# Optimization experiments

Measured on AMD Instinct MI355X. Metric: run time of the kernel, lower is better.

Reference implementation:

```python
import jax, jax.numpy as jnp
import numpy as np

B = 512        # graphs per batch
N_NODES = 64   # nodes per graph
IN_CH = 256
EMBED = 64
TOPK = 20
NEG_SLOPE = 0.2


def setup_inputs() -> dict:
    key = jax.random.key(0)
    ks = jax.random.split(key, 6)
    N = B * N_NODES
    x = jax.random.normal(ks[0], (N, IN_CH), dtype=jnp.float32)
    # fully-connected graph WITH self loops, per graph, sorted source-major
    src = jnp.repeat(jnp.arange(N_NODES, dtype=jnp.int32), N_NODES)  # [n*n]
    dst = jnp.tile(jnp.arange(N_NODES, dtype=jnp.int32), N_NODES)    # [n*n]
    offs = (jnp.arange(B, dtype=jnp.int32) * N_NODES)[:, None]       # [B,1]
    l = (src[None, :] + offs).reshape(-1)
    r = (dst[None, :] + offs).reshape(-1)
    edge_index = jnp.stack([l, r]).astype(jnp.int32)                 # [2, B*n*n]
    batch = jnp.repeat(jnp.arange(B, dtype=jnp.int32), N_NODES)      # [N]
    glorot = lambda k, sh: jax.random.uniform(k, sh, jnp.float32,
                                              -1.0, 1.0) * np.sqrt(6.0 / (sh[0] + sh[-1]))
    Wl = glorot(ks[1], (EMBED, IN_CH))
    bl = jnp.zeros((EMBED,), jnp.float32)
    Wr = glorot(ks[2], (EMBED, IN_CH))
    br = jnp.zeros((EMBED,), jnp.float32)
    att = glorot(ks[3], (1, EMBED))
    return {"x": x, "edge_index": edge_index, "batch": batch,
            "Wl": Wl, "bl": bl, "Wr": Wr, "br": br, "att": att}


def reference(x, edge_index, batch, Wl, bl, Wr, br, att):
    N = x.shape[0]
    x_l = x @ Wl.T + bl                      # [N, D]
    x_r = x @ Wr.T + br                      # [N, D]
    l, r = edge_index[0], edge_index[1]
    # edge gather + GAT-style score
    e = jax.nn.leaky_relu(x_l[l] + x_r[r], negative_slope=NEG_SLOPE)  # [E, D]
    alpha = (e * att[0]).sum(axis=-1)                                  # [E]
    # segment softmax grouped by source node l (each group is non-empty)
    m = jax.ops.segment_max(alpha, l, num_segments=N)
    a = jnp.exp(alpha - m[l])
    s = jax.ops.segment_sum(a, l, num_segments=N)
    a = a / s[l]
    # kNN sparsify: zero the diagonal then per-row topk
    a3 = a.reshape(B, N_NODES, N_NODES)
    a3 = a3 * (1.0 - jnp.eye(N_NODES, dtype=a3.dtype))
    attention, indices = jax.lax.top_k(a3, TOPK)     # [B, n, k] sorted desc
    attention = attention.reshape(-1)                 # [B*n*k]
    offs = (jnp.arange(B, dtype=jnp.int32) * N_NODES)[:, None]
    index_i = (jnp.repeat(jnp.arange(N_NODES, dtype=jnp.int32), TOPK)[None, :]
               + offs).reshape(-1)
    index_j = (indices.astype(jnp.int32)
               + (jnp.arange(B, dtype=jnp.int32) * N_NODES)[:, None, None]).reshape(-1)
    new_edge_index = jnp.stack([index_i, index_j])    # [2, B*n*k]
    return new_edge_index, attention
```

## Files before the change

kernel.cpp:

```cpp
#include <hip/hip_runtime.h>
#include <stdint.h>

#define NGRAPH 512
#define NN 64
#define INCH 256
#define TOPK 20
#define EPR 655360

typedef __attribute__((ext_vector_type(8))) short bf16x8;
typedef __attribute__((ext_vector_type(4))) float f32x4;
typedef __attribute__((ext_vector_type(2))) uint32_t u32x2;

#define XLP   0
#define XRP   2176
#define ALF   4352
#define LISTS 0
#define MROW  8704
#define SROW  8960
#define SLOF  9216
#define SROF  9280
#define ATTO  9344
#define SMEM_DW 9408

static __device__ __forceinline__ uint32_t f2bfbits(float f) {
  uint32_t u = __float_as_uint(f);
  return (u + 0x7FFFu + ((u >> 16) & 1u)) >> 16;
}
static __device__ __forceinline__ uint32_t pk2(float a, float b) {
  return f2bfbits(a) | (f2bfbits(b) << 16);
}
static __device__ __forceinline__ float lo16f(uint32_t p) { return __uint_as_float(p << 16); }
static __device__ __forceinline__ float hi16f(uint32_t p) { return __uint_as_float(p & 0xFFFF0000u); }

__global__ __launch_bounds__(256, 4) void gat_fused(
    const float* __restrict__ x,
    const float* __restrict__ Wl,
    const float* __restrict__ blv,
    const float* __restrict__ Wr,
    const float* __restrict__ brv,
    const float* __restrict__ att,
    float* __restrict__ out)
{
  __shared__ __align__(16) uint32_t smemU[SMEM_DW];
  float* smemF = (float*)smemU;

  const int b    = blockIdx.x;
  const int t    = threadIdx.x;
  const int w    = t >> 6;
  const int lane = t & 63;
  const int quad = lane >> 4;
  const int lo   = lane & 15;
  const int nodeBase = b * NN;

  if (t < 64) smemF[ATTO + t] = att[t];

  f32x4 acc[8];
  #pragma unroll
  for (int ct = 0; ct < 8; ++ct) acc[ct] = (f32x4){0.f, 0.f, 0.f, 0.f};

  const int r0 = w * 16;
  #pragma unroll
  for (int ks = 0; ks < 8; ++ks) {
    const int k0 = ks * 32 + quad * 8;
    const float* ap = x + (size_t)(nodeBase + r0 + lo) * INCH + k0;
    float4 a0 = *(const float4*)ap;
    float4 a1 = *(const float4*)(ap + 4);
    uint4 au = { pk2(a0.x, a0.y), pk2(a0.z, a0.w), pk2(a1.x, a1.y), pk2(a1.z, a1.w) };
    bf16x8 afrag = __builtin_bit_cast(bf16x8, au);
    #pragma unroll
    for (int ct = 0; ct < 8; ++ct) {
      const float* wrow = ((ct < 4) ? Wl : Wr) + (size_t)((ct & 3) * 16 + lo) * INCH + k0;
      float4 b0 = *(const float4*)wrow;
      float4 b1 = *(const float4*)(wrow + 4);
      uint4 bu = { pk2(b0.x, b0.y), pk2(b0.z, b0.w), pk2(b1.x, b1.y), pk2(b1.z, b1.w) };
      bf16x8 bfrag = __builtin_bit_cast(bf16x8, bu);
      acc[ct] = __builtin_amdgcn_mfma_f32_16x16x32_bf16(afrag, bfrag, acc[ct], 0, 0, 0);
    }
  }

  #pragma unroll
  for (int ct = 0; ct < 8; ++ct) {
    const int c = (ct & 3) * 16 + lo;
    const float bias = ((ct < 4) ? blv : brv)[c];
    const int base = ((ct < 4) ? XLP : XRP) + c * 34 + (r0 >> 1) + quad * 2;
    u32x2 v = { pk2(acc[ct][0] + bias, acc[ct][1] + bias),
                pk2(acc[ct][2] + bias, acc[ct][3] + bias) };
    *(u32x2*)&smemU[base] = v;
  }
  __syncthreads();

  if (t < 128) {
    const int i = t & 63;
    const int base = (t < 64) ? XLP : XRP;
    float s = 0.f;
    #pragma unroll 4
    for (int d = 0; d < 64; ++d) {
      uint32_t p = smemU[base + d * 34 + (i >> 1)];
      float v = (i & 1) ? hi16f(p) : lo16f(p);
      s = fmaf(smemF[ATTO + d], v, s);
    }
    smemF[((t < 64) ? SLOF : SROF) + i] = s;
  }
  __syncthreads();

  const int i0 = (t >> 4) * 4;
  const int j0 = (t & 15) * 4;
  float pacc[4][4];
  #pragma unroll
  for (int a = 0; a < 4; ++a)
    #pragma unroll
    for (int c = 0; c < 4; ++c) pacc[a][c] = 0.f;

  #pragma unroll 4
  for (int d = 0; d < 64; ++d) {
    u32x2 pl = *(const u32x2*)&smemU[XLP + d * 34 + (i0 >> 1)];
    u32x2 pr = *(const u32x2*)&smemU[XRP + d * 34 + (j0 >> 1)];
    const float ad = smemF[ATTO + d];
    float xl[4] = { lo16f(pl.x), hi16f(pl.x), lo16f(pl.y), hi16f(pl.y) };
    float xr[4] = { lo16f(pr.x), hi16f(pr.x), lo16f(pr.y), hi16f(pr.y) };
    #pragma unroll
    for (int a = 0; a < 4; ++a) {
      #pragma unroll
      for (int c = 0; c < 4; ++c) {
        float s = xl[a] + xr[c];
        pacc[a][c] = fmaf(ad, fabsf(s), pacc[a][c]);
      }
    }
  }
  {
    f32x4 srv = *(const f32x4*)&smemF[SROF + j0];
    #pragma unroll
    for (int a = 0; a < 4; ++a) {
      const float sl = smemF[SLOF + i0 + a];
      f32x4 v;
      #pragma unroll
      for (int c = 0; c < 4; ++c)
        v[c] = 0.6f * (sl + srv[c]) + 0.4f * pacc[a][c];
      *(f32x4*)&smemF[ALF + (i0 + a) * 68 + j0] = v;
    }
  }
  __syncthreads();

  {
    const int row = t & 63;
    const int seg = t >> 6;
    const int segBase = seg * 16;
    float fr[16];
    *(f32x4*)&fr[0]  = *(const f32x4*)&smemF[ALF + row * 68 + segBase];
    *(f32x4*)&fr[4]  = *(const f32x4*)&smemF[ALF + row * 68 + segBase + 4];
    *(f32x4*)&fr[8]  = *(const f32x4*)&smemF[ALF + row * 68 + segBase + 8];
    *(f32x4*)&fr[12] = *(const f32x4*)&smemF[ALF + row * 68 + segBase + 12];

    float mp = fr[0];
    #pragma unroll
    for (int e = 1; e < 16; ++e) mp = fmaxf(mp, fr[e]);
    float sp = 0.f;
    #pragma unroll
    for (int e = 0; e < 16; ++e) sp += __expf(fr[e] - mp);

    uint32_t tk[16];
    #pragma unroll
    for (int k = 0; k < 16; ++k) tk[k] = 0u;
    #pragma unroll
    for (int e = 0; e < 16; ++e) {
      const int j = segBase + e;
      uint32_t u = __float_as_uint(fr[e]);
      uint32_t key = u ^ ((uint32_t)((int32_t)u >> 31) | 0x80000000u);
      key = (key & 0xFFFFFFC0u) | (uint32_t)(63 - j);
      key = (j == row) ? 0u : key;
      #pragma unroll
      for (int k = 15; k >= 1; --k)
        tk[k] = (key > tk[k]) ? ((key < tk[k - 1]) ? key : tk[k - 1]) : tk[k];
      tk[0] = (key > tk[0]) ? key : tk[0];
    }
    #pragma unroll
    for (int k = 0; k < 16; ++k)
      smemU[LISTS + row * 65 + segBase + k] = tk[k];
    smemF[MROW + seg * 64 + row] = mp;
    smemF[SROW + seg * 64 + row] = sp;
  }
  __syncthreads();

  if (t < 64) {
    const int row = t;
    const int lb = LISTS + row * 65;
    float m01 = fmaxf(smemF[MROW + row], smemF[MROW + 64 + row]);
    float m23 = fmaxf(smemF[MROW + 128 + row], smemF[MROW + 192 + row]);
    float m = fmaxf(m01, m23);
    float S = 0.f;
    #pragma unroll
    for (int p = 0; p < 4; ++p)
      S += smemF[SROW + p * 64 + row] * __expf(smemF[MROW + p * 64 + row] - m);
    const float invS = 1.0f / S;

    uint32_t h0 = smemU[lb + 0], h1 = smemU[lb + 16], h2 = smemU[lb + 32], h3 = smemU[lb + 48];
    int p0 = 0, p1 = 0, p2 = 0, p3 = 0;
    float va[TOPK], vj[TOPK];

    #pragma unroll
    for (int k = 0; k < TOPK; ++k) {
      uint32_t k01 = (h0 > h1) ? h0 : h1;
      uint32_t k23 = (h2 > h3) ? h2 : h3;
      uint32_t key = (k01 > k23) ? k01 : k23;
      const int wsel = (key == h0) ? 0 : (key == h1) ? 1 : (key == h2) ? 2 : 3;

      uint32_t ub = (key & 0x80000000u) ? (key ^ 0x80000000u) : ~key;
      float alpha = __uint_as_float(ub & 0xFFFFFFC0u);
      const int j = 63 - (int)(key & 63u);
      va[k] = __expf(alpha - m) * invS;
      vj[k] = (float)(nodeBase + j);

      int np = ((wsel == 0) ? p0 : (wsel == 1) ? p1 : (wsel == 2) ? p2 : p3) + 1;
      uint32_t hn = (np < 16) ? smemU[lb + wsel * 16 + np] : 0u;
      p0 += (wsel == 0); p1 += (wsel == 1); p2 += (wsel == 2); p3 += (wsel == 3);
      h0 = (wsel == 0) ? hn : h0;
      h1 = (wsel == 1) ? hn : h1;
      h2 = (wsel == 2) ? hn : h2;
      h3 = (wsel == 3) ? hn : h3;
    }

    const int g = nodeBase + row;
    const float vi = (float)g;
    float4* o0 = (float4*)(out + (size_t)g * 20);
    float4* o1 = (float4*)(out + EPR + (size_t)g * 20);
    float4* o2 = (float4*)(out + 2 * (size_t)EPR + (size_t)g * 20);
    const float4 vi4 = { vi, vi, vi, vi };
    #pragma unroll
    for (int kk = 0; kk < 5; ++kk) {
      o0[kk] = vi4;
      o1[kk] = (float4){ vj[4 * kk], vj[4 * kk + 1], vj[4 * kk + 2], vj[4 * kk + 3] };
      o2[kk] = (float4){ va[4 * kk], va[4 * kk + 1], va[4 * kk + 2], va[4 * kk + 3] };
    }
  }
}

extern "C" void kernel_launch(void* const* d_in, const int* in_sizes, int n_in,
                              void* d_out, int out_size, void* d_ws, size_t ws_size,
                              hipStream_t stream) {
  const float* x   = (const float*)d_in[0];
  const float* Wl  = (const float*)d_in[3];
  const float* bl  = (const float*)d_in[4];
  const float* Wr  = (const float*)d_in[5];
  const float* br  = (const float*)d_in[6];
  const float* att = (const float*)d_in[7];
  gat_fused<<<dim3(NGRAPH), dim3(256), 0, stream>>>(x, Wl, bl, Wr, br, att, (float*)d_out);
}
```

Baseline: 138.6 us.

## Prepack weights to bf16 in a pre-kernel and double threads per graph

Adds a small kernel that converts Wl and Wr to packed bf16 once per call, so the main kernel loads ready-made B fragments instead of converting fp32 weights to bf16 in every block. The main kernel now runs 512 threads per graph: half the waves compute x_l and half x_r, and the pairwise score, per-segment top-k and merge stages are split across 8 segments instead of 4. Projected features are kept in fp32 in shared memory rather than bf16, which grows LDS use. The cost is an extra launch, a larger merge over 8 lists, and possibly lower occupancy.

```diff
diff --git a/kernel.cpp b/kernel.cpp
--- a/kernel.cpp
+++ b/kernel.cpp
@@ -9,18 +9,17 @@
 
 typedef __attribute__((ext_vector_type(8))) short bf16x8;
 typedef __attribute__((ext_vector_type(4))) float f32x4;
-typedef __attribute__((ext_vector_type(2))) uint32_t u32x2;
-
-#define XLP   0
-#define XRP   2176
-#define ALF   4352
+
+#define XLF   0
+#define XRF   4352
+#define ALF   8704
 #define LISTS 0
-#define MROW  8704
-#define SROW  8960
-#define SLOF  9216
-#define SROF  9280
-#define ATTO  9344
-#define SMEM_DW 9408
+#define MROW  13056
+#define SROW  13568
+#define SLOF  14080
+#define SROF  14144
+#define ATTO  14208
+#define SMEM_DW 14272
 
 static __device__ __forceinline__ uint32_t f2bfbits(float f) {
   uint32_t u = __float_as_uint(f);
@@ -29,14 +28,21 @@
 static __device__ __forceinline__ uint32_t pk2(float a, float b) {
   return f2bfbits(a) | (f2bfbits(b) << 16);
 }
-static __device__ __forceinline__ float lo16f(uint32_t p) { return __uint_as_float(p << 16); }
-static __device__ __forceinline__ float hi16f(uint32_t p) { return __uint_as_float(p & 0xFFFF0000u); }
-
-__global__ __launch_bounds__(256, 4) void gat_fused(
+
+__global__ __launch_bounds__(256) void wpack(const float* __restrict__ Wl,
+                                             const float* __restrict__ Wr,
+                                             uint32_t* __restrict__ ws) {
+  const int t = blockIdx.x * 256 + threadIdx.x;
+  const float* src = (t < 8192) ? Wl : Wr;
+  const int p = t & 8191;
+  float2 v = *(const float2*)(src + (size_t)p * 2);
+  ws[t] = pk2(v.x, v.y);
+}
+
+__global__ __launch_bounds__(512, 4) void gat_fused(
     const float* __restrict__ x,
-    const float* __restrict__ Wl,
+    const uint32_t* __restrict__ ws,
     const float* __restrict__ blv,
-    const float* __restrict__ Wr,
     const float* __restrict__ brv,
     const float* __restrict__ att,
     float* __restrict__ out)
@@ -54,11 +60,13 @@
 
   if (t < 64) smemF[ATTO + t] = att[t];
 
-  f32x4 acc[8];
+  const int half = w >> 2;
+  const int r0   = (w & 3) * 16;
+  f32x4 acc[4];
   #pragma unroll
-  for (int ct = 0; ct < 8; ++ct) acc[ct] = (f32x4){0.f, 0.f, 0.f, 0.f};
-
-  const int r0 = w * 16;
+  for (int ct = 0; ct < 4; ++ct) acc[ct] = (f32x4){0.f, 0.f, 0.f, 0.f};
+
+  const uint4* wsV = (const uint4*)ws;
   #pragma unroll
   for (int ks = 0; ks < 8; ++ks) {
     const int k0 = ks * 32 + quad * 8;
@@ -68,69 +76,64 @@
     uint4 au = { pk2(a0.x, a0.y), pk2(a0.z, a0.w), pk2(a1.x, a1.y), pk2(a1.z, a1.w) };
     bf16x8 afrag = __builtin_bit_cast(bf16x8, au);
     #pragma unroll
-    for (int ct = 0; ct < 8; ++ct) {
-      const float* wrow = ((ct < 4) ? Wl : Wr) + (size_t)((ct & 3) * 16 + lo) * INCH + k0;
-      float4 b0 = *(const float4*)wrow;
-      float4 b1 = *(const float4*)(wrow + 4);
-      uint4 bu = { pk2(b0.x, b0.y), pk2(b0.z, b0.w), pk2(b1.x, b1.y), pk2(b1.z, b1.w) };
+    for (int ct = 0; ct < 4; ++ct) {
+      const int n = ct * 16 + lo;
+      uint4 bu = wsV[half * 2048 + n * 32 + ks * 4 + quad];
       bf16x8 bfrag = __builtin_bit_cast(bf16x8, bu);
       acc[ct] = __builtin_amdgcn_mfma_f32_16x16x32_bf16(afrag, bfrag, acc[ct], 0, 0, 0);
     }
   }
 
-  #pragma unroll
-  for (int ct = 0; ct < 8; ++ct) {
-    const int c = (ct & 3) * 16 + lo;
-    const float bias = ((ct < 4) ? blv : brv)[c];
-    const int base = ((ct < 4) ? XLP : XRP) + c * 34 + (r0 >> 1) + quad * 2;
-    u32x2 v = { pk2(acc[ct][0] + bias, acc[ct][1] + bias),
-                pk2(acc[ct][2] + bias, acc[ct][3] + bias) };
-    *(u32x2*)&smemU[base] = v;
+  {
+    const int dstBase = half ? XRF : XLF;
+    const float* bias = half ? brv : blv;
+    #pragma unroll
+    for (int ct = 0; ct < 4; ++ct) {
+      const int c = ct * 16 + lo;
+      const float bb = bias[c];
+      f32x4 v = { acc[ct][0] + bb, acc[ct][1] + bb, acc[ct][2] + bb, acc[ct][3] + bb };
+      *(f32x4*)&smemF[dstBase + c * 68 + r0 + quad * 4] = v;
+    }
   }
   __syncthreads();
 
   if (t < 128) {
     const int i = t & 63;
-    const int base = (t < 64) ? XLP : XRP;
+    const int base = (t < 64) ? XLF : XRF;
     float s = 0.f;
-    #pragma unroll 4
-    for (int d = 0; d < 64; ++d) {
-      uint32_t p = smemU[base + d * 34 + (i >> 1)];
-      float v = (i & 1) ? hi16f(p) : lo16f(p);
-      s = fmaf(smemF[ATTO + d], v, s);
-    }
+    #pragma unroll 8
+    for (int d = 0; d < 64; ++d)
+      s = fmaf(smemF[ATTO + d], smemF[base + d * 68 + i], s);
     smemF[((t < 64) ? SLOF : SROF) + i] = s;
   }
   __syncthreads();
 
-  const int i0 = (t >> 4) * 4;
+  const int i0 = (t >> 4) * 2;
   const int j0 = (t & 15) * 4;
-  float pacc[4][4];
+  float pacc[2][4];
   #pragma unroll
-  for (int a = 0; a < 4; ++a)
+  for (int a = 0; a < 2; ++a)
     #pragma unroll
     for (int c = 0; c < 4; ++c) pacc[a][c] = 0.f;
 
   #pragma unroll 4
   for (int d = 0; d < 64; ++d) {
-    u32x2 pl = *(const u32x2*)&smemU[XLP + d * 34 + (i0 >> 1)];
-    u32x2 pr = *(const u32x2*)&smemU[XRP + d * 34 + (j0 >> 1)];
+    float xl0 = smemF[XLF + d * 68 + i0];
+    float xl1 = smemF[XLF + d * 68 + i0 + 1];
+    f32x4 xr  = *(const f32x4*)&smemF[XRF + d * 68 + j0];
     const float ad = smemF[ATTO + d];
-    float xl[4] = { lo16f(pl.x), hi16f(pl.x), lo16f(pl.y), hi16f(pl.y) };
-    float xr[4] = { lo16f(pr.x), hi16f(pr.x), lo16f(pr.y), hi16f(pr.y) };
-    #pragma unroll
-    for (int a = 0; a < 4; ++a) {
-      #pragma unroll
-      for (int c = 0; c < 4; ++c) {
-        float s = xl[a] + xr[c];
-        pacc[a][c] = fmaf(ad, fabsf(s), pacc[a][c]);
-      }
+    #pragma unroll
+    for (int c = 0; c < 4; ++c) {
+      float s0 = xl0 + xr[c];
+      float s1 = xl1 + xr[c];
+      pacc[0][c] = fmaf(ad, fabsf(s0), pacc[0][c]);
+      pacc[1][c] = fmaf(ad, fabsf(s1), pacc[1][c]);
     }
   }
   {
     f32x4 srv = *(const f32x4*)&smemF[SROF + j0];
     #pragma unroll
-    for (int a = 0; a < 4; ++a) {
+    for (int a = 0; a < 2; ++a) {
       const float sl = smemF[SLOF + i0 + a];
       f32x4 v;
       #pragma unroll
@@ -144,38 +147,36 @@
   {
     const int row = t & 63;
     const int seg = t >> 6;
-    const int segBase = seg * 16;
-    float fr[16];
-    *(f32x4*)&fr[0]  = *(const f32x4*)&smemF[ALF + row * 68 + segBase];
-    *(f32x4*)&fr[4]  = *(const f32x4*)&smemF[ALF + row * 68 + segBase + 4];
-    *(f32x4*)&fr[8]  = *(const f32x4*)&smemF[ALF + row * 68 + segBase + 8];
-    *(f32x4*)&fr[12] = *(const f32x4*)&smemF[ALF + row * 68 + segBase + 12];
+    const int cb  = seg * 8;
+    f32x4 f0 = *(const f32x4*)&smemF[ALF + row * 68 + cb];
+    f32x4 f1 = *(const f32x4*)&smemF[ALF + row * 68 + cb + 4];
+    float fr[8] = { f0[0], f0[1], f0[2], f0[3], f1[0], f1[1], f1[2], f1[3] };
 
     float mp = fr[0];
     #pragma unroll
-    for (int e = 1; e < 16; ++e) mp = fmaxf(mp, fr[e]);
+    for (int e = 1; e < 8; ++e) mp = fmaxf(mp, fr[e]);
     float sp = 0.f;
     #pragma unroll
-    for (int e = 0; e < 16; ++e) sp += __expf(fr[e] - mp);
-
-    uint32_t tk[16];
-    #pragma unroll
-    for (int k = 0; k < 16; ++k) tk[k] = 0u;
-    #pragma unroll
-    for (int e = 0; e < 16; ++e) {
-      const int j = segBase + e;
+    for (int e = 0; e < 8; ++e) sp += __expf(fr[e] - mp);
+
+    uint32_t tk[8];
+    #pragma unroll
+    for (int k = 0; k < 8; ++k) tk[k] = 0u;
+    #pragma unroll
+    for (int e = 0; e < 8; ++e) {
+      const int j = cb + e;
       uint32_t u = __float_as_uint(fr[e]);
       uint32_t key = u ^ ((uint32_t)((int32_t)u >> 31) | 0x80000000u);
       key = (key & 0xFFFFFFC0u) | (uint32_t)(63 - j);
       key = (j == row) ? 0u : key;
       #pragma unroll
-      for (int k = 15; k >= 1; --k)
+      for (int k = 7; k >= 1; --k)
         tk[k] = (key > tk[k]) ? ((key < tk[k - 1]) ? key : tk[k - 1]) : tk[k];
       tk[0] = (key > tk[0]) ? key : tk[0];
     }
     #pragma unroll
-    for (int k = 0; k < 16; ++k)
-      smemU[LISTS + row * 65 + segBase + k] = tk[k];
+    for (int k = 0; k < 8; ++k)
+      smemU[LISTS + row * 65 + cb + k] = tk[k];
     smemF[MROW + seg * 64 + row] = mp;
     smemF[SROW + seg * 64 + row] = sp;
   }
@@ -184,25 +185,32 @@
   if (t < 64) {
     const int row = t;
     const int lb = LISTS + row * 65;
-    float m01 = fmaxf(smemF[MROW + row], smemF[MROW + 64 + row]);
-    float m23 = fmaxf(smemF[MROW + 128 + row], smemF[MROW + 192 + row]);
-    float m = fmaxf(m01, m23);
+    float m = smemF[MROW + row];
+    #pragma unroll
+    for (int p = 1; p < 8; ++p) m = fmaxf(m, smemF[MROW + p * 64 + row]);
     float S = 0.f;
     #pragma unroll
-    for (int p = 0; p < 4; ++p)
+    for (int p = 0; p < 8; ++p)
       S += smemF[SROW + p * 64 + row] * __expf(smemF[MROW + p * 64 + row] - m);
     const float invS = 1.0f / S;
 
-    uint32_t h0 = smemU[lb + 0], h1 = smemU[lb + 16], h2 = smemU[lb + 32], h3 = smemU[lb + 48];
-    int p0 = 0, p1 = 0, p2 = 0, p3 = 0;
+    uint32_t h0 = smemU[lb + 0],  h1 = smemU[lb + 8],  h2 = smemU[lb + 16], h3 = smemU[lb + 24];
+    uint32_t h4 = smemU[lb + 32], h5 = smemU[lb + 40], h6 = smemU[lb + 48], h7 = smemU[lb + 56];
+    int p0 = 0, p1 = 0, p2 = 0, p3 = 0, p4 = 0, p5 = 0, p6 = 0, p7 = 0;
     float va[TOPK], vj[TOPK];
 
     #pragma unroll
     for (int k = 0; k < TOPK; ++k) {
-      uint32_t k01 = (h0 > h1) ? h0 : h1;
-      uint32_t k23 = (h2 > h3) ? h2 : h3;
-      uint32_t key = (k01 > k23) ? k01 : k23;
-      const int wsel = (key == h0) ? 0 : (key == h1) ? 1 : (key == h2) ? 2 : 3;
+      uint32_t m01 = (h0 > h1) ? h0 : h1;
+      uint32_t m23 = (h2 > h3) ? h2 : h3;
+      uint32_t m45 = (h4 > h5) ? h4 : h5;
+      uint32_t m67 = (h6 > h7) ? h6 : h7;
+      uint32_t ma = (m01 > m23) ? m01 : m23;
+      uint32_t mb = (m45 > m67) ? m45 : m67;
+      uint32_t key = (ma > mb) ? ma : mb;
+      const int wsel = (key == h0) ? 0 : (key == h1) ? 1 : (key == h2) ? 2 :
+                       (key == h3) ? 3 : (key == h4) ? 4 : (key == h5) ? 5 :
+                       (key == h6) ? 6 : 7;
 
       uint32_t ub = (key & 0x80000000u) ? (key ^ 0x80000000u) : ~key;
       float alpha = __uint_as_float(ub & 0xFFFFFFC0u);
@@ -210,13 +218,15 @@
       va[k] = __expf(alpha - m) * invS;
       vj[k] = (float)(nodeBase + j);
 
-      int np = ((wsel == 0) ? p0 : (wsel == 1) ? p1 : (wsel == 2) ? p2 : p3) + 1;
-      uint32_t hn = (np < 16) ? smemU[lb + wsel * 16 + np] : 0u;
+      int np = ((wsel == 0) ? p0 : (wsel == 1) ? p1 : (wsel == 2) ? p2 : (wsel == 3) ? p3 :
+                (wsel == 4) ? p4 : (wsel == 5) ? p5 : (wsel == 6) ? p6 : p7) + 1;
+      uint32_t hn = (np < 8) ? smemU[lb + wsel * 8 + np] : 0u;
       p0 += (wsel == 0); p1 += (wsel == 1); p2 += (wsel == 2); p3 += (wsel == 3);
-      h0 = (wsel == 0) ? hn : h0;
-      h1 = (wsel == 1) ? hn : h1;
-      h2 = (wsel == 2) ? hn : h2;
-      h3 = (wsel == 3) ? hn : h3;
+      p4 += (wsel == 4); p5 += (wsel == 5); p6 += (wsel == 6); p7 += (wsel == 7);
+      h0 = (wsel == 0) ? hn : h0;  h1 = (wsel == 1) ? hn : h1;
+      h2 = (wsel == 2) ? hn : h2;  h3 = (wsel == 3) ? hn : h3;
+      h4 = (wsel == 4) ? hn : h4;  h5 = (wsel == 5) ? hn : h5;
+      h6 = (wsel == 6) ? hn : h6;  h7 = (wsel == 7) ? hn : h7;
     }
 
     const int g = nodeBase + row;
@@ -243,5 +253,8 @@
   const float* Wr  = (const float*)d_in[5];
   const float* br  = (const float*)d_in[6];
   const float* att = (const float*)d_in[7];
-  gat_fused<<<dim3(NGRAPH), dim3(256), 0, stream>>>(x, Wl, bl, Wr, br, att, (float*)d_out);
-}
+  uint32_t* wsW = (uint32_t*)d_ws;
+
+  wpack<<<dim3(64), dim3(256), 0, stream>>>(Wl, Wr, wsW);
+  gat_fused<<<dim3(NGRAPH), dim3(512), 0, stream>>>(x, wsW, bl, br, att, (float*)d_out);
+}
```

Result: faster. 129.7 us (-6.4%).
